# Optimization experiments

Measured on AMD Instinct MI355X. Metric: run time of the kernel, lower is better.

Reference implementation:

```python
import jax, jax.numpy as jnp
import numpy as np

B, S, D, H, HD = 2, 4096, 768, 12, 64
W = 256  # one-sided attention window (attention_window=512 // 2)
SCALE = 1.0 / np.sqrt(HD).astype(np.float32)
NEG = -1e9


def setup_inputs() -> dict:
    key = jax.random.key(0)
    ks = jax.random.split(key, 13)
    inp = {"hidden_states": jax.random.normal(ks[0], (B, S, D), dtype=jnp.float32)}
    names = ["Wq", "Wk", "Wv", "Wqg", "Wkg", "Wvg"]
    for i, n in enumerate(names):
        inp[n] = jax.random.normal(ks[1 + i], (D, D), dtype=jnp.float32) * 0.02
        inp["b" + n[1:]] = jax.random.normal(ks[7 + i], (D,), dtype=jnp.float32) * 0.02
    inp["num_global"] = 32
    return inp


def _heads(x):
    # [B,S,D] -> [B,H,S,HD]
    return x.reshape(B, S, H, HD).transpose(0, 2, 1, 3)


def longformer_attn(hidden_states, Wq, bq, Wk, bk, Wv, bv, Wqg, bqg, Wkg, bkg, Wvg, bvg, G):
    q = _heads(hidden_states @ Wq + bq) * SCALE
    k = _heads(hidden_states @ Wk + bk)
    v = _heads(hidden_states @ Wv + bv)

    nc = S // W  # number of query chunks
    # --- banded (sliding window) scores via overlapping key chunks of size 3W ---
    Qc = q.reshape(B, H, nc, W, HD)
    kpad = jnp.pad(k, ((0, 0), (0, 0), (W, W), (0, 0)))
    win_idx = jnp.arange(nc)[:, None] * W + jnp.arange(3 * W)[None, :]  # [nc, 3W]
    K3 = kpad[:, :, win_idx]  # [B,H,nc,3W,HD]
    band = jnp.einsum('bhcqd,bhckd->bhcqk', Qc, K3)  # [B,H,nc,W,3W]
    # mask: key abs position in range, and relative offset within [-W, W]
    c = jnp.arange(nc)[:, None, None]
    pq = jnp.arange(W)[None, :, None]
    e = jnp.arange(3 * W)[None, None, :]
    kabs = c * W + e - W
    valid = (kabs >= 0) & (kabs < S) & (e >= pq) & (e <= pq + 2 * W)
    band = jnp.where(valid[None, None], band, NEG).reshape(B, H, S, 3 * W)

    # --- all queries also attend to the G global keys (regular key proj) ---
    sg = jnp.einsum('bhsd,bhgd->bhsg', q, k[:, :, :G])  # [B,H,S,G]
    probs = jax.nn.softmax(jnp.concatenate([sg, band], axis=-1), axis=-1)
    pg, pb = probs[..., :G], probs[..., G:].reshape(B, H, nc, W, 3 * W)

    vpad = jnp.pad(v, ((0, 0), (0, 0), (W, W), (0, 0)))
    V3 = vpad[:, :, win_idx]  # [B,H,nc,3W,HD]
    out = jnp.einsum('bhcqk,bhckd->bhcqd', pb, V3).reshape(B, H, S, HD)
    out = out + jnp.einsum('bhsg,bhgd->bhsd', pg, v[:, :, :G])

    # --- global queries attend to ALL tokens with the *_global projections ---
    qg = _heads(hidden_states @ Wqg + bqg)[:, :, :G] * SCALE  # [B,H,G,HD]
    kgf = _heads(hidden_states @ Wkg + bkg)
    vgf = _heads(hidden_states @ Wvg + bvg)
    gp = jax.nn.softmax(jnp.einsum('bhgd,bhsd->bhgs', qg, kgf), axis=-1)
    gout = jnp.einsum('bhgs,bhsd->bhgd', gp, vgf)  # [B,H,G,HD]
    out = out.at[:, :, :G].set(gout)

    return out.transpose(0, 2, 1, 3).reshape(B, S, D)


def reference(hidden_states, Wq, bq, Wk, bk, Wv, bv, Wqg, bqg, Wkg, bkg, Wvg, bvg, num_global):
    return longformer_attn(hidden_states, Wq, bq, Wk, bk, Wv, bv, Wqg, bqg, Wkg, bkg, Wvg, bvg, int(num_global))
```

## Files before the change

### kernel.cpp

```cpp
#include <hip/hip_runtime.h>
#include <hip/hip_bf16.h>


#define DEVI __device__ __forceinline__
typedef _Float16 f16;
typedef _Float16 h4 __attribute__((ext_vector_type(4)));
typedef _Float16 f16x8 __attribute__((ext_vector_type(8)));
typedef __attribute__((ext_vector_type(4))) float float4v;

DEVI float4v mfma16(f16x8 a, f16x8 b, float4v c) {
    return __builtin_amdgcn_mfma_f32_16x16x32_f16(a, b, c, 0, 0, 0);
}

DEVI void gl_lds16(const f16* g, f16* l) {
    __builtin_amdgcn_global_load_lds(
        (const __attribute__((address_space(1))) unsigned int*)g,
        (__attribute__((address_space(3))) unsigned int*)l, 16, 0, 0);
}

__global__ __launch_bounds__(256) void prep(
    const float* __restrict__ x,
    const float* __restrict__ w0, const float* __restrict__ w1,
    const float* __restrict__ w2, const float* __restrict__ w3,
    const float* __restrict__ w4, const float* __restrict__ w5,
    f16* __restrict__ xh, f16* __restrict__ wt) {
    __shared__ float tile[64][65];
    int bid = blockIdx.x;
    if (bid < 6144) {
        int i = (bid * 256 + threadIdx.x) * 4;
        float4 v = *(const float4*)&x[i];
        h4 o = {(f16)v.x, (f16)v.y, (f16)v.z, (f16)v.w};
        *(h4*)&xh[i] = o;
    } else {
        int t = bid - 6144;
        int i = t / 144, rem = t - i * 144;
        int n0 = (rem % 12) * 64, k0 = (rem / 12) * 64;
        const float* W = (i == 0) ? w0 : (i == 1) ? w1 : (i == 2) ? w2
                       : (i == 3) ? w3 : (i == 4) ? w4 : w5;
        int tx = threadIdx.x & 63, ty = threadIdx.x >> 6;
#pragma unroll
        for (int yy = 0; yy < 64; yy += 4)
            tile[yy + ty][tx] = W[(size_t)(k0 + yy + ty) * 768 + n0 + tx];
        __syncthreads();
#pragma unroll
        for (int yy = 0; yy < 64; yy += 4)
            wt[(size_t)(i * 768 + n0 + yy + ty) * 768 + k0 + tx] = (f16)tile[tx][yy + ty];
    }
}

__global__ __launch_bounds__(256, 2) void qkv_mfma11(
    const f16* __restrict__ Xh, const f16* __restrict__ Wt,
    const float* __restrict__ b0, const float* __restrict__ b1,
    const float* __restrict__ b2, const float* __restrict__ b3,
    const float* __restrict__ b4, const float* __restrict__ b5,
    f16* __restrict__ q, f16* __restrict__ k, f16* __restrict__ vT,
    f16* __restrict__ qg, f16* __restrict__ kg, f16* __restrict__ vgT) {
    __shared__ __align__(16) char smem[73728];
    f16* As = (f16*)smem;
    f16* Bs = (f16*)(smem + 24576);
    f16* Cl = (f16*)smem;

    int tid = threadIdx.x, lane = tid & 63, wid = tid >> 6;
    int quad = lane >> 4, l15 = lane & 15;

    int L = blockIdx.x + (blockIdx.y << 6);
    int xcd = L & 7, W = L >> 3;
    int mt = xcd * 8 + (W & 7);
    int yy = W >> 3;
    int m0 = mt * 128;
    int grp = yy / 3;
    if (grp == 3 && (m0 & 4095) != 0) return;
    int nb = (yy - grp * 3) * 256;
    int wm = (wid >> 1) * 64;
    int wn = (wid & 1) * 128;
    const f16* arow0 = Xh + (size_t)m0 * 768;
    const f16* brow0 = Wt + (size_t)(grp * 768 + nb) * 768;

    float4v acc[4][8];
#pragma unroll
    for (int i = 0; i < 4; ++i)
#pragma unroll
        for (int j = 0; j < 8; ++j) acc[i][j] = (float4v){0.f, 0.f, 0.f, 0.f};

    int r0 = tid >> 2;
    int o0 = (((tid & 3) ^ ((r0 >> 1) & 3)) << 3);
    int sw8 = ((quad ^ ((l15 >> 1) & 3)) << 3);

    auto STAGE_T = [&](int kt, int buf) {
        int k0 = kt << 5;
        const f16* ag = &arow0[(size_t)r0 * 768 + k0 + o0];
        const f16* bg = &brow0[(size_t)r0 * 768 + k0 + o0];
        f16* al = As + buf * 4096 + wid * 512;
        f16* bl = Bs + buf * 8192 + wid * 512;
        gl_lds16(ag, al);
        gl_lds16(ag + (size_t)64 * 768, al + 2048);
        gl_lds16(bg, bl);
        gl_lds16(bg + (size_t)64 * 768, bl + 2048);
        gl_lds16(bg + (size_t)128 * 768, bl + 4096);
        gl_lds16(bg + (size_t)192 * 768, bl + 6144);
    };

    auto COMPUTE_T = [&](int t) {
        const f16* Ab = As + (t % 3) * 4096;
        const f16* Bb = Bs + (t % 3) * 8192;
        f16x8 af[4], bf[8];
#pragma unroll
        for (int i = 0; i < 4; ++i)
            af[i] = *(const f16x8*)&Ab[(wm + i * 16 + l15) * 32 + sw8];
#pragma unroll
        for (int j = 0; j < 8; ++j)
            bf[j] = *(const f16x8*)&Bb[(wn + j * 16 + l15) * 32 + sw8];
        __builtin_amdgcn_s_setprio(1);
#pragma unroll
        for (int i = 0; i < 4; ++i)
#pragma unroll
            for (int j = 0; j < 8; ++j)
                acc[i][j] = mfma16(af[i], bf[j], acc[i][j]);
        __builtin_amdgcn_s_setprio(0);
    };

    STAGE_T(0, 0);
    STAGE_T(1, 1);
#pragma unroll
    for (int t = 0; t < 24; ++t) {
        if (t < 23) {
            asm volatile("s_waitcnt vmcnt(6)" ::: "memory");
        } else {
            asm volatile("s_waitcnt vmcnt(0)" ::: "memory");
        }
        __builtin_amdgcn_s_barrier();
        __builtin_amdgcn_sched_barrier(0);
        if (t + 2 <= 23) STAGE_T(t + 2, (t + 2) % 3);
        COMPUTE_T(t);
    }
    __syncthreads();

    const float* Bsel = (grp == 0) ? b0 : (grp == 1) ? b1 : (grp == 2) ? b2
                      : (grp == 3) ? b3 : (grp == 4) ? b4 : b5;
    int b = m0 >> 12;
    bool tr = (grp == 2 || grp == 5);

    if (tr) {
        constexpr int CLD2 = 136;
#pragma unroll
        for (int j = 0; j < 8; ++j) {
            float bias = Bsel[nb + wn + j * 16 + l15];
#pragma unroll
            for (int i = 0; i < 4; ++i) {
                float4v a = acc[i][j];
                h4 pk = {(f16)(a[0] + bias), (f16)(a[1] + bias),
                         (f16)(a[2] + bias), (f16)(a[3] + bias)};
                *(h4*)&Cl[(wn + j * 16 + l15) * CLD2 + wm + i * 16 + quad * 4] = pk;
            }
        }
        __syncthreads();
        f16* base = (grp == 2) ? vT : vgT;
        int c = tid;
        int ncol = nb + c, h = ncol >> 6, hd = ncol & 63;
        f16* dst = &base[((size_t)((b * 12 + h) * 64 + hd)) * 4096 + (m0 & 4095)];
        const f16* src = &Cl[c * CLD2];
#pragma unroll
        for (int ii = 0; ii < 16; ++ii)
            *(f16x8*)&dst[ii * 8] = *(const f16x8*)&src[ii * 8];
    } else {
        constexpr int CLD = 264;
        float scale = (grp == 0 || grp == 3) ? 0.125f : 1.0f;
#pragma unroll
        for (int j = 0; j < 8; ++j) {
            float bias = Bsel[nb + wn + j * 16 + l15];
#pragma unroll
            for (int i = 0; i < 4; ++i) {
                float4v a = acc[i][j];
#pragma unroll
                for (int r = 0; r < 4; ++r)
                    Cl[(wm + i * 16 + quad * 4 + r) * CLD + wn + j * 16 + l15] =
                        (f16)((a[r] + bias) * scale);
            }
        }
        __syncthreads();
        int row = tid & 127, half = tid >> 7;
        int s = (m0 & 4095) + row;
        const f16* src = &Cl[row * CLD + half * 128];
        if (grp == 3) {
            if (s < 32) {
#pragma unroll
                for (int ii = 0; ii < 16; ++ii) {
                    int h = (nb >> 6) + (half << 1) + (ii >> 3), hd = (ii & 7) * 8;
                    *(f16x8*)&qg[((size_t)((b * 12 + h) * 32 + s)) * 64 + hd] =
                        *(const f16x8*)&src[ii * 8];
                }
            }
        } else {
            f16* baseb = (grp == 0) ? q : (grp == 1) ? k : kg;
#pragma unroll
            for (int ii = 0; ii < 16; ++ii) {
                int h = (nb >> 6) + (half << 1) + (ii >> 3), hd = (ii & 7) * 8;
                *(f16x8*)&baseb[((size_t)((b * 12 + h) * 4096 + s)) * 64 + hd] =
                    *(const f16x8*)&src[ii * 8];
            }
        }
    }
}

__global__ __launch_bounds__(256, 3) void band_mfma5b(
    const f16* __restrict__ q, const f16* __restrict__ k, const f16* __restrict__ vT,
    float* __restrict__ out) {
    constexpr int LDK = 72, LDV = 136, LDP = 40;
    __shared__ __align__(16) f16 Kt[128 * LDK];
    __shared__ __align__(16) f16 Vt[64 * LDV];
    __shared__ __align__(16) f16 Pt[4][32 * LDP];
    int tid = threadIdx.x, lane = tid & 63, wid = tid >> 6;
    int quad = lane >> 4, l15 = lane & 15;
    int L = blockIdx.x;
    int c = (L & 7) * 4 + ((L >> 3) & 3);
    int bh = L >> 5;
    int h = bh % 12, b = bh / 12;
    const f16* qsl = q + (size_t)(b * 12 + h) * 4096 * 64;
    const f16* ksl = k + (size_t)(b * 12 + h) * 4096 * 64;
    const f16* vsl = vT + (size_t)(b * 12 + h) * 64 * 4096;
    int q0 = c * 128;
    int pq0 = q0 + wid * 32;

    f16x8 qf[2][2];
#pragma unroll
    for (int qg = 0; qg < 2; ++qg)
#pragma unroll
        for (int ks = 0; ks < 2; ++ks)
            qf[qg][ks] = *(const f16x8*)&qsl[(size_t)(pq0 + qg * 16 + l15) * 64 +
                                             ks * 32 + quad * 8];

    float4v Ot[4][2];
#pragma unroll
    for (int dt = 0; dt < 4; ++dt)
#pragma unroll
        for (int qg = 0; qg < 2; ++qg) Ot[dt][qg] = (float4v){0.f, 0.f, 0.f, 0.f};
    float lacc[2] = {0.f, 0.f};
    f16* PW = &Pt[wid][0];

    {
#pragma unroll
        for (int jt = 0; jt < 2; ++jt) {
            f16x8 kf0 = *(const f16x8*)&ksl[(size_t)(jt * 16 + l15) * 64 + quad * 8];
            f16x8 kf1 = *(const f16x8*)&ksl[(size_t)(jt * 16 + l15) * 64 + 32 + quad * 8];
#pragma unroll
            for (int qg = 0; qg < 2; ++qg) {
                float4v sacc = (float4v){0.f, 0.f, 0.f, 0.f};
                sacc = mfma16(kf0, qf[qg][0], sacc);
                sacc = mfma16(kf1, qf[qg][1], sacc);
                float p0 = __expf(sacc[0]), p1 = __expf(sacc[1]);
                float p2 = __expf(sacc[2]), p3 = __expf(sacc[3]);
                lacc[qg] += (p0 + p1) + (p2 + p3);
                h4 pk = {(f16)p0, (f16)p1, (f16)p2, (f16)p3};
                *(h4*)&PW[(qg * 16 + l15) * LDP + jt * 16 + quad * 4] = pk;
            }
        }
        f16x8 pf0 = *(const f16x8*)&PW[l15 * LDP + quad * 8];
        f16x8 pf1 = *(const f16x8*)&PW[(16 + l15) * LDP + quad * 8];
#pragma unroll
        for (int dt = 0; dt < 4; ++dt) {
            f16x8 vf = *(const f16x8*)&vsl[(size_t)(dt * 16 + l15) * 4096 + quad * 8];
            Ot[dt][0] = mfma16(vf, pf0, Ot[dt][0]);
            Ot[dt][1] = mfma16(vf, pf1, Ot[dt][1]);
        }
    }

    for (int r = 0; r < 5; ++r) {
        int kb = q0 - 256 + r * 128;
        if (kb < 0 || kb >= 4096) continue;
        __syncthreads();
        {
            int kr = tid >> 1, ko = (tid & 1) * 32;
            const f16* ks2 = &ksl[(size_t)(kb + kr) * 64 + ko];
            f16* kd = &Kt[kr * LDK + ko];
#pragma unroll
            for (int i = 0; i < 4; ++i) *(f16x8*)&kd[i * 8] = *(const f16x8*)&ks2[i * 8];
            int vr = tid >> 2, vo = (tid & 3) * 32;
            const f16* vs2 = &vsl[(size_t)vr * 4096 + kb + vo];
            f16* vd = &Vt[vr * LDV + vo];
#pragma unroll
            for (int i = 0; i < 4; ++i) *(f16x8*)&vd[i * 8] = *(const f16x8*)&vs2[i * 8];
        }
        __syncthreads();

        if (kb + 127 < pq0 - 256 || kb > pq0 + 287) continue;

#pragma unroll
        for (int tt = 0; tt < 2; ++tt) {
            int tb = kb + tt * 64;
            if (tb + 63 < pq0 - 256 || tb > pq0 + 287) continue;
#pragma unroll
            for (int hf = 0; hf < 2; ++hf) {
#pragma unroll
                for (int jt = 0; jt < 2; ++jt) {
                    int jl = tt * 64 + hf * 32 + jt * 16;
                    f16x8 kf0 = *(const f16x8*)&Kt[(jl + l15) * LDK + quad * 8];
                    f16x8 kf1 = *(const f16x8*)&Kt[(jl + l15) * LDK + 32 + quad * 8];
                    int j0 = kb + jl;
#pragma unroll
                    for (int qg = 0; qg < 2; ++qg) {
                        int qlo = pq0 + qg * 16;
                        h4 pk = {(f16)0.f, (f16)0.f, (f16)0.f, (f16)0.f};
                        bool dead = (j0 < qlo - 271) || (j0 > qlo + 271);
                        if (!dead) {
                            float4v sacc = (float4v){0.f, 0.f, 0.f, 0.f};
                            sacc = mfma16(kf0, qf[qg][0], sacc);
                            sacc = mfma16(kf1, qf[qg][1], sacc);
                            float p[4];
                            bool full = (j0 >= qlo - 241) && (j0 <= qlo + 241);
                            if (full) {
#pragma unroll
                                for (int rr = 0; rr < 4; ++rr) p[rr] = __expf(sacc[rr]);
                            } else {
#pragma unroll
                                for (int rr = 0; rr < 4; ++rr) {
                                    int d = (j0 + quad * 4 + rr) - (qlo + l15);
                                    p[rr] = ((unsigned)(d + 256) <= 512u) ? __expf(sacc[rr]) : 0.f;
                                }
                            }
                            lacc[qg] += (p[0] + p[1]) + (p[2] + p[3]);
                            pk = (h4){(f16)p[0], (f16)p[1], (f16)p[2], (f16)p[3]};
                        }
                        *(h4*)&PW[(qg * 16 + l15) * LDP + jt * 16 + quad * 4] = pk;
                    }
                }
                f16x8 pf0 = *(const f16x8*)&PW[l15 * LDP + quad * 8];
                f16x8 pf1 = *(const f16x8*)&PW[(16 + l15) * LDP + quad * 8];
#pragma unroll
                for (int dt = 0; dt < 4; ++dt) {
                    f16x8 vf = *(const f16x8*)&Vt[(dt * 16 + l15) * LDV +
                                                  tt * 64 + hf * 32 + quad * 8];
                    Ot[dt][0] = mfma16(vf, pf0, Ot[dt][0]);
                    Ot[dt][1] = mfma16(vf, pf1, Ot[dt][1]);
                }
            }
        }
    }

#pragma unroll
    for (int qg = 0; qg < 2; ++qg) {
        float lsum = lacc[qg];
        lsum += __shfl_xor(lsum, 16);
        lsum += __shfl_xor(lsum, 32);
        float inv = 1.f / lsum;
        size_t orow = (size_t)(b * 4096 + pq0 + qg * 16 + l15) * 768 + h * 64;
#pragma unroll
        for (int dt = 0; dt < 4; ++dt) {
            float4 o4 = {Ot[dt][qg][0] * inv, Ot[dt][qg][1] * inv,
                         Ot[dt][qg][2] * inv, Ot[dt][qg][3] * inv};
            *(float4*)&out[orow + dt * 16 + quad * 4] = o4;
        }
    }
}

__global__ __launch_bounds__(256) void global_part(
    const f16* __restrict__ qg, const f16* __restrict__ kg, const f16* __restrict__ vgT,
    float* __restrict__ Opart, float* __restrict__ Lpart) {
    constexpr int LDP = 72;
    __shared__ __align__(16) f16 Pt[4][32 * LDP];
    __shared__ __align__(16) float Osh[4][64 * 32];
    __shared__ float Lsh[4][32];
    int tid = threadIdx.x, lane = tid & 63, wid = tid >> 6;
    int quad = lane >> 4, l15 = lane & 15;
    int sl = blockIdx.x & 7, bh = blockIdx.x >> 3;
    const f16* qsl = qg + (size_t)bh * 32 * 64;
    const f16* ksl = kg + (size_t)bh * 4096 * 64;
    const f16* vsl = vgT + (size_t)bh * 64 * 4096;
    int kbase = sl * 512 + wid * 128;

    f16x8 qf[2][2];
#pragma unroll
    for (int g = 0; g < 2; ++g)
#pragma unroll
        for (int ks = 0; ks < 2; ++ks)
            qf[g][ks] = *(const f16x8*)&qsl[(size_t)(g * 16 + l15) * 64 + ks * 32 + quad * 8];

    float4v Ot[4][2];
#pragma unroll
    for (int dt = 0; dt < 4; ++dt)
#pragma unroll
        for (int g = 0; g < 2; ++g) Ot[dt][g] = (float4v){0.f, 0.f, 0.f, 0.f};
    float lacc[2] = {0.f, 0.f};
    f16* PW = &Pt[wid][0];

#pragma unroll
    for (int hf = 0; hf < 2; ++hf) {
        int kh0 = kbase + hf * 64;
#pragma unroll
        for (int kt = 0; kt < 4; ++kt) {
            int jb = kh0 + kt * 16;
            f16x8 kf0 = *(const f16x8*)&ksl[(size_t)(jb + l15) * 64 + quad * 8];
            f16x8 kf1 = *(const f16x8*)&ksl[(size_t)(jb + l15) * 64 + 32 + quad * 8];
#pragma unroll
            for (int g = 0; g < 2; ++g) {
                float4v sacc = (float4v){0.f, 0.f, 0.f, 0.f};
                sacc = mfma16(kf0, qf[g][0], sacc);
                sacc = mfma16(kf1, qf[g][1], sacc);
                float p0 = __expf(sacc[0]), p1 = __expf(sacc[1]);
                float p2 = __expf(sacc[2]), p3 = __expf(sacc[3]);
                lacc[g] += (p0 + p1) + (p2 + p3);
                h4 pk = {(f16)p0, (f16)p1, (f16)p2, (f16)p3};
                *(h4*)&PW[(g * 16 + l15) * LDP + kt * 16 + quad * 4] = pk;
            }
        }
#pragma unroll
        for (int kh = 0; kh < 2; ++kh) {
            f16x8 pf0 = *(const f16x8*)&PW[l15 * LDP + kh * 32 + quad * 8];
            f16x8 pf1 = *(const f16x8*)&PW[(16 + l15) * LDP + kh * 32 + quad * 8];
#pragma unroll
            for (int dt = 0; dt < 4; ++dt) {
                f16x8 vf = *(const f16x8*)&vsl[(size_t)(dt * 16 + l15) * 4096 +
                                               kh0 + kh * 32 + quad * 8];
                Ot[dt][0] = mfma16(vf, pf0, Ot[dt][0]);
                Ot[dt][1] = mfma16(vf, pf1, Ot[dt][1]);
            }
        }
    }

#pragma unroll
    for (int g = 0; g < 2; ++g) {
        lacc[g] += __shfl_xor(lacc[g], 16);
        lacc[g] += __shfl_xor(lacc[g], 32);
    }
    if (quad == 0) { Lsh[wid][l15] = lacc[0]; Lsh[wid][16 + l15] = lacc[1]; }
#pragma unroll
    for (int dt = 0; dt < 4; ++dt)
#pragma unroll
        for (int g = 0; g < 2; ++g)
#pragma unroll
            for (int r = 0; r < 4; ++r)
                Osh[wid][(dt * 16 + quad * 4 + r) * 32 + g * 16 + l15] = Ot[dt][g][r];
    __syncthreads();
#pragma unroll
    for (int i = 0; i < 8; ++i) {
        int idx = tid + i * 256;
        int d = idx & 63, qq = idx >> 6;
        float v = Osh[0][d * 32 + qq] + Osh[1][d * 32 + qq] +
                  Osh[2][d * 32 + qq] + Osh[3][d * 32 + qq];
        Opart[(size_t)blockIdx.x * 2048 + idx] = v;
    }
    if (tid < 32)
        Lpart[blockIdx.x * 32 + tid] = Lsh[0][tid] + Lsh[1][tid] + Lsh[2][tid] + Lsh[3][tid];
}

__global__ __launch_bounds__(256) void global_reduce(
    const float* __restrict__ Opart, const float* __restrict__ Lpart,
    float* __restrict__ out) {
    __shared__ float Ls[32];
    int tid = threadIdx.x, bh = blockIdx.x;
    int b = bh / 12, h = bh % 12;
    if (tid < 32) {
        float s = 0.f;
#pragma unroll
        for (int sl = 0; sl < 8; ++sl) s += Lpart[(bh * 8 + sl) * 32 + tid];
        Ls[tid] = s;
    }
    __syncthreads();
#pragma unroll
    for (int i = 0; i < 8; ++i) {
        int idx = tid + i * 256;
        int d = idx & 63, qq = idx >> 6;
        float o = 0.f;
#pragma unroll
        for (int sl = 0; sl < 8; ++sl) o += Opart[(size_t)(bh * 8 + sl) * 2048 + idx];
        out[(size_t)(b * 4096 + qq) * 768 + h * 64 + d] = o / Ls[qq];
    }
}

extern "C" void kernel_launch(void* const* d_in, const int* in_sizes, int n_in,
                              void* d_out, int out_size, void* d_ws, size_t ws_size,
                              hipStream_t stream) {
    const float* hs = (const float*)d_in[0];
    float* outp = (float*)d_out;

    char* p = (char*)d_ws;
    const size_t SLAB = (size_t)2 * 12 * 4096 * 64 * sizeof(f16);
    f16* qb   = (f16*)(p + 0 * SLAB);
    f16* kb   = (f16*)(p + 1 * SLAB);
    f16* vtb  = (f16*)(p + 2 * SLAB);
    f16* kgb  = (f16*)(p + 3 * SLAB);
    f16* vgtb = (f16*)(p + 4 * SLAB);
    f16* qgb  = (f16*)(p + 5 * SLAB);
    char* p2  = p + 5 * SLAB + 196608;
    f16* xh   = (f16*)p2;
    f16* wt   = (f16*)(p2 + SLAB);
    char* p3  = p2 + SLAB + 7077888;
    float* Opart = (float*)p3;
    float* Lpart = (float*)(p3 + 1572864);

    prep<<<7008, 256, 0, stream>>>(
        hs,
        (const float*)d_in[1], (const float*)d_in[3], (const float*)d_in[5],
        (const float*)d_in[7], (const float*)d_in[9], (const float*)d_in[11],
        xh, wt);
    qkv_mfma11<<<dim3(64, 18), 256, 0, stream>>>(
        xh, wt,
        (const float*)d_in[2], (const float*)d_in[4], (const float*)d_in[6],
        (const float*)d_in[8], (const float*)d_in[10], (const float*)d_in[12],
        qb, kb, vtb, qgb, kgb, vgtb);
    band_mfma5b<<<768, 256, 0, stream>>>(qb, kb, vtb, outp);
    global_part<<<192, 256, 0, stream>>>(qgb, kgb, vgtb, Opart, Lpart);
    global_reduce<<<24, 256, 0, stream>>>(Opart, Lpart, outp);
}
```

Measured before the change: 227.2 us.

## Fuse band attention and global-query partial kernels into one launch

Merges the sliding-window band kernel and the global-query partial kernel into a single 960-block launch, branching on block index and sharing one LDS buffer. The aim is to save a kernel launch and let the 192 global blocks fill the tail of the band grid. The band block index mapping also changes from the interleaved chunk order to a linear one, which changes cache locality. The shared LDS allocation is sized for the larger global path (about 51 KB), which may lower band-block occupancy compared to its own smaller footprint.

```diff
diff --git a/kernel.cpp b/kernel.cpp
--- a/kernel.cpp
+++ b/kernel.cpp
@@ -202,244 +202,240 @@
     }
 }
 
-__global__ __launch_bounds__(256, 3) void band_mfma5b(
+__global__ __launch_bounds__(256, 3) void band_global(
     const f16* __restrict__ q, const f16* __restrict__ k, const f16* __restrict__ vT,
-    float* __restrict__ out) {
-    constexpr int LDK = 72, LDV = 136, LDP = 40;
-    __shared__ __align__(16) f16 Kt[128 * LDK];
-    __shared__ __align__(16) f16 Vt[64 * LDV];
-    __shared__ __align__(16) f16 Pt[4][32 * LDP];
+    const f16* __restrict__ qg, const f16* __restrict__ kg, const f16* __restrict__ vgT,
+    float* __restrict__ out, float* __restrict__ Opart, float* __restrict__ Lpart) {
+    __shared__ __align__(16) char smem[51712];
     int tid = threadIdx.x, lane = tid & 63, wid = tid >> 6;
     int quad = lane >> 4, l15 = lane & 15;
-    int L = blockIdx.x;
-    int c = (L & 7) * 4 + ((L >> 3) & 3);
-    int bh = L >> 5;
-    int h = bh % 12, b = bh / 12;
-    const f16* qsl = q + (size_t)(b * 12 + h) * 4096 * 64;
-    const f16* ksl = k + (size_t)(b * 12 + h) * 4096 * 64;
-    const f16* vsl = vT + (size_t)(b * 12 + h) * 64 * 4096;
-    int q0 = c * 128;
-    int pq0 = q0 + wid * 32;
-
-    f16x8 qf[2][2];
-#pragma unroll
-    for (int qg = 0; qg < 2; ++qg)
-#pragma unroll
-        for (int ks = 0; ks < 2; ++ks)
-            qf[qg][ks] = *(const f16x8*)&qsl[(size_t)(pq0 + qg * 16 + l15) * 64 +
-                                             ks * 32 + quad * 8];
-
-    float4v Ot[4][2];
-#pragma unroll
-    for (int dt = 0; dt < 4; ++dt)
-#pragma unroll
-        for (int qg = 0; qg < 2; ++qg) Ot[dt][qg] = (float4v){0.f, 0.f, 0.f, 0.f};
-    float lacc[2] = {0.f, 0.f};
-    f16* PW = &Pt[wid][0];
-
-    {
-#pragma unroll
-        for (int jt = 0; jt < 2; ++jt) {
-            f16x8 kf0 = *(const f16x8*)&ksl[(size_t)(jt * 16 + l15) * 64 + quad * 8];
-            f16x8 kf1 = *(const f16x8*)&ksl[(size_t)(jt * 16 + l15) * 64 + 32 + quad * 8];
-#pragma unroll
-            for (int qg = 0; qg < 2; ++qg) {
-                float4v sacc = (float4v){0.f, 0.f, 0.f, 0.f};
-                sacc = mfma16(kf0, qf[qg][0], sacc);
-                sacc = mfma16(kf1, qf[qg][1], sacc);
-                float p0 = __expf(sacc[0]), p1 = __expf(sacc[1]);
-                float p2 = __expf(sacc[2]), p3 = __expf(sacc[3]);
-                lacc[qg] += (p0 + p1) + (p2 + p3);
-                h4 pk = {(f16)p0, (f16)p1, (f16)p2, (f16)p3};
-                *(h4*)&PW[(qg * 16 + l15) * LDP + jt * 16 + quad * 4] = pk;
-            }
-        }
-        f16x8 pf0 = *(const f16x8*)&PW[l15 * LDP + quad * 8];
-        f16x8 pf1 = *(const f16x8*)&PW[(16 + l15) * LDP + quad * 8];
-#pragma unroll
-        for (int dt = 0; dt < 4; ++dt) {
-            f16x8 vf = *(const f16x8*)&vsl[(size_t)(dt * 16 + l15) * 4096 + quad * 8];
-            Ot[dt][0] = mfma16(vf, pf0, Ot[dt][0]);
-            Ot[dt][1] = mfma16(vf, pf1, Ot[dt][1]);
-        }
-    }
-
-    for (int r = 0; r < 5; ++r) {
-        int kb = q0 - 256 + r * 128;
-        if (kb < 0 || kb >= 4096) continue;
-        __syncthreads();
+
+    if (blockIdx.x < 768) {
+        constexpr int LDK = 72, LDV = 136, LDP = 40;
+        f16* Kt = (f16*)smem;
+        f16* Vt = (f16*)(smem + 18432);
+        f16* PW = (f16*)(smem + 35840) + wid * 32 * LDP;
+        int c = blockIdx.x & 31, h = (blockIdx.x >> 5) % 12, b = blockIdx.x / 384;
+        const f16* qsl = q + (size_t)(b * 12 + h) * 4096 * 64;
+        const f16* ksl = k + (size_t)(b * 12 + h) * 4096 * 64;
+        const f16* vsl = vT + (size_t)(b * 12 + h) * 64 * 4096;
+        int q0 = c * 128;
+        int pq0 = q0 + wid * 32;
+
+        f16x8 qf[2][2];
+#pragma unroll
+        for (int qg2 = 0; qg2 < 2; ++qg2)
+#pragma unroll
+            for (int ks = 0; ks < 2; ++ks)
+                qf[qg2][ks] = *(const f16x8*)&qsl[(size_t)(pq0 + qg2 * 16 + l15) * 64 +
+                                                  ks * 32 + quad * 8];
+
+        float4v Ot[4][2];
+#pragma unroll
+        for (int dt = 0; dt < 4; ++dt)
+#pragma unroll
+            for (int qg2 = 0; qg2 < 2; ++qg2) Ot[dt][qg2] = (float4v){0.f, 0.f, 0.f, 0.f};
+        float lacc[2] = {0.f, 0.f};
+
         {
-            int kr = tid >> 1, ko = (tid & 1) * 32;
-            const f16* ks2 = &ksl[(size_t)(kb + kr) * 64 + ko];
-            f16* kd = &Kt[kr * LDK + ko];
-#pragma unroll
-            for (int i = 0; i < 4; ++i) *(f16x8*)&kd[i * 8] = *(const f16x8*)&ks2[i * 8];
-            int vr = tid >> 2, vo = (tid & 3) * 32;
-            const f16* vs2 = &vsl[(size_t)vr * 4096 + kb + vo];
-            f16* vd = &Vt[vr * LDV + vo];
-#pragma unroll
-            for (int i = 0; i < 4; ++i) *(f16x8*)&vd[i * 8] = *(const f16x8*)&vs2[i * 8];
-        }
-        __syncthreads();
-
-        if (kb + 127 < pq0 - 256 || kb > pq0 + 287) continue;
-
-#pragma unroll
-        for (int tt = 0; tt < 2; ++tt) {
-            int tb = kb + tt * 64;
-            if (tb + 63 < pq0 - 256 || tb > pq0 + 287) continue;
-#pragma unroll
-            for (int hf = 0; hf < 2; ++hf) {
-#pragma unroll
-                for (int jt = 0; jt < 2; ++jt) {
-                    int jl = tt * 64 + hf * 32 + jt * 16;
-                    f16x8 kf0 = *(const f16x8*)&Kt[(jl + l15) * LDK + quad * 8];
-                    f16x8 kf1 = *(const f16x8*)&Kt[(jl + l15) * LDK + 32 + quad * 8];
-                    int j0 = kb + jl;
-#pragma unroll
-                    for (int qg = 0; qg < 2; ++qg) {
-                        int qlo = pq0 + qg * 16;
-                        h4 pk = {(f16)0.f, (f16)0.f, (f16)0.f, (f16)0.f};
-                        bool dead = (j0 < qlo - 271) || (j0 > qlo + 271);
-                        if (!dead) {
-                            float4v sacc = (float4v){0.f, 0.f, 0.f, 0.f};
-                            sacc = mfma16(kf0, qf[qg][0], sacc);
-                            sacc = mfma16(kf1, qf[qg][1], sacc);
-                            float p[4];
-                            bool full = (j0 >= qlo - 241) && (j0 <= qlo + 241);
-                            if (full) {
-#pragma unroll
-                                for (int rr = 0; rr < 4; ++rr) p[rr] = __expf(sacc[rr]);
-                            } else {
-#pragma unroll
-                                for (int rr = 0; rr < 4; ++rr) {
-                                    int d = (j0 + quad * 4 + rr) - (qlo + l15);
-                                    p[rr] = ((unsigned)(d + 256) <= 512u) ? __expf(sacc[rr]) : 0.f;
+#pragma unroll
+            for (int jt = 0; jt < 2; ++jt) {
+                f16x8 kf0 = *(const f16x8*)&ksl[(size_t)(jt * 16 + l15) * 64 + quad * 8];
+                f16x8 kf1 = *(const f16x8*)&ksl[(size_t)(jt * 16 + l15) * 64 + 32 + quad * 8];
+#pragma unroll
+                for (int qg2 = 0; qg2 < 2; ++qg2) {
+                    float4v sacc = (float4v){0.f, 0.f, 0.f, 0.f};
+                    sacc = mfma16(kf0, qf[qg2][0], sacc);
+                    sacc = mfma16(kf1, qf[qg2][1], sacc);
+                    float p0 = __expf(sacc[0]), p1 = __expf(sacc[1]);
+                    float p2 = __expf(sacc[2]), p3 = __expf(sacc[3]);
+                    lacc[qg2] += (p0 + p1) + (p2 + p3);
+                    h4 pk = {(f16)p0, (f16)p1, (f16)p2, (f16)p3};
+                    *(h4*)&PW[(qg2 * 16 + l15) * LDP + jt * 16 + quad * 4] = pk;
+                }
+            }
+            f16x8 pf0 = *(const f16x8*)&PW[l15 * LDP + quad * 8];
+            f16x8 pf1 = *(const f16x8*)&PW[(16 + l15) * LDP + quad * 8];
+#pragma unroll
+            for (int dt = 0; dt < 4; ++dt) {
+                f16x8 vf = *(const f16x8*)&vsl[(size_t)(dt * 16 + l15) * 4096 + quad * 8];
+                Ot[dt][0] = mfma16(vf, pf0, Ot[dt][0]);
+                Ot[dt][1] = mfma16(vf, pf1, Ot[dt][1]);
+            }
+        }
+
+        for (int r = 0; r < 5; ++r) {
+            int kb = q0 - 256 + r * 128;
+            if (kb < 0 || kb >= 4096) continue;
+            __syncthreads();
+            {
+                int kr = tid >> 1, ko = (tid & 1) * 32;
+                const f16* ks2 = &ksl[(size_t)(kb + kr) * 64 + ko];
+                f16* kd = &Kt[kr * LDK + ko];
+#pragma unroll
+                for (int i = 0; i < 4; ++i) *(f16x8*)&kd[i * 8] = *(const f16x8*)&ks2[i * 8];
+                int vr = tid >> 2, vo = (tid & 3) * 32;
+                const f16* vs2 = &vsl[(size_t)vr * 4096 + kb + vo];
+                f16* vd = &Vt[vr * LDV + vo];
+#pragma unroll
+                for (int i = 0; i < 4; ++i) *(f16x8*)&vd[i * 8] = *(const f16x8*)&vs2[i * 8];
+            }
+            __syncthreads();
+
+            if (kb + 127 < pq0 - 256 || kb > pq0 + 287) continue;
+
+#pragma unroll
+            for (int tt = 0; tt < 2; ++tt) {
+                int tb = kb + tt * 64;
+                if (tb + 63 < pq0 - 256 || tb > pq0 + 287) continue;
+#pragma unroll
+                for (int hf = 0; hf < 2; ++hf) {
+#pragma unroll
+                    for (int jt = 0; jt < 2; ++jt) {
+                        int jl = tt * 64 + hf * 32 + jt * 16;
+                        f16x8 kf0 = *(const f16x8*)&Kt[(jl + l15) * LDK + quad * 8];
+                        f16x8 kf1 = *(const f16x8*)&Kt[(jl + l15) * LDK + 32 + quad * 8];
+                        int j0 = kb + jl;
+#pragma unroll
+                        for (int qg2 = 0; qg2 < 2; ++qg2) {
+                            int qlo = pq0 + qg2 * 16;
+                            h4 pk = {(f16)0.f, (f16)0.f, (f16)0.f, (f16)0.f};
+                            bool dead = (j0 < qlo - 271) || (j0 > qlo + 271);
+                            if (!dead) {
+                                float4v sacc = (float4v){0.f, 0.f, 0.f, 0.f};
+                                sacc = mfma16(kf0, qf[qg2][0], sacc);
+                                sacc = mfma16(kf1, qf[qg2][1], sacc);
+                                float p[4];
+                                bool full = (j0 >= qlo - 241) && (j0 <= qlo + 241);
+                                if (full) {
+#pragma unroll
+                                    for (int rr = 0; rr < 4; ++rr) p[rr] = __expf(sacc[rr]);
+                                } else {
+#pragma unroll
+                                    for (int rr = 0; rr < 4; ++rr) {
+                                        int d = (j0 + quad * 4 + rr) - (qlo + l15);
+                                        p[rr] = ((unsigned)(d + 256) <= 512u) ? __expf(sacc[rr]) : 0.f;
+                                    }
                                 }
+                                lacc[qg2] += (p[0] + p[1]) + (p[2] + p[3]);
+                                pk = (h4){(f16)p[0], (f16)p[1], (f16)p[2], (f16)p[3]};
                             }
-                            lacc[qg] += (p[0] + p[1]) + (p[2] + p[3]);
-                            pk = (h4){(f16)p[0], (f16)p[1], (f16)p[2], (f16)p[3]};
+                            *(h4*)&PW[(qg2 * 16 + l15) * LDP + jt * 16 + quad * 4] = pk;
                         }
-                        *(h4*)&PW[(qg * 16 + l15) * LDP + jt * 16 + quad * 4] = pk;
+                    }
+                    f16x8 pf0 = *(const f16x8*)&PW[l15 * LDP + quad * 8];
+                    f16x8 pf1 = *(const f16x8*)&PW[(16 + l15) * LDP + quad * 8];
+#pragma unroll
+                    for (int dt = 0; dt < 4; ++dt) {
+                        f16x8 vf = *(const f16x8*)&Vt[(dt * 16 + l15) * LDV +
+                                                      tt * 64 + hf * 32 + quad * 8];
+                        Ot[dt][0] = mfma16(vf, pf0, Ot[dt][0]);
+                        Ot[dt][1] = mfma16(vf, pf1, Ot[dt][1]);
                     }
                 }
-                f16x8 pf0 = *(const f16x8*)&PW[l15 * LDP + quad * 8];
-                f16x8 pf1 = *(const f16x8*)&PW[(16 + l15) * LDP + quad * 8];
+            }
+        }
+
+#pragma unroll
+        for (int qg2 = 0; qg2 < 2; ++qg2) {
+            float lsum = lacc[qg2];
+            lsum += __shfl_xor(lsum, 16);
+            lsum += __shfl_xor(lsum, 32);
+            float inv = 1.f / lsum;
+            size_t orow = (size_t)(b * 4096 + pq0 + qg2 * 16 + l15) * 768 + h * 64;
+#pragma unroll
+            for (int dt = 0; dt < 4; ++dt) {
+                float4 o4 = {Ot[dt][qg2][0] * inv, Ot[dt][qg2][1] * inv,
+                             Ot[dt][qg2][2] * inv, Ot[dt][qg2][3] * inv};
+                *(float4*)&out[orow + dt * 16 + quad * 4] = o4;
+            }
+        }
+    } else {
+        constexpr int LDP = 72;
+        f16* PW = (f16*)smem + wid * 32 * LDP;
+        float* Osh = (float*)(smem + 18432);
+        float* Lsh = (float*)(smem + 18432 + 32768);
+        int bid = blockIdx.x - 768;
+        int sl = bid & 7, bh = bid >> 3;
+        const f16* qsl = qg + (size_t)bh * 32 * 64;
+        const f16* ksl = kg + (size_t)bh * 4096 * 64;
+        const f16* vsl = vgT + (size_t)bh * 64 * 4096;
+        int kbase = sl * 512 + wid * 128;
+
+        f16x8 qf[2][2];
+#pragma unroll
+        for (int g = 0; g < 2; ++g)
+#pragma unroll
+            for (int ks = 0; ks < 2; ++ks)
+                qf[g][ks] = *(const f16x8*)&qsl[(size_t)(g * 16 + l15) * 64 + ks * 32 + quad * 8];
+
+        float4v Ot[4][2];
+#pragma unroll
+        for (int dt = 0; dt < 4; ++dt)
+#pragma unroll
+            for (int g = 0; g < 2; ++g) Ot[dt][g] = (float4v){0.f, 0.f, 0.f, 0.f};
+        float lacc[2] = {0.f, 0.f};
+
+#pragma unroll
+        for (int hf = 0; hf < 2; ++hf) {
+            int kh0 = kbase + hf * 64;
+#pragma unroll
+            for (int kt = 0; kt < 4; ++kt) {
+                int jb = kh0 + kt * 16;
+                f16x8 kf0 = *(const f16x8*)&ksl[(size_t)(jb + l15) * 64 + quad * 8];
+                f16x8 kf1 = *(const f16x8*)&ksl[(size_t)(jb + l15) * 64 + 32 + quad * 8];
+#pragma unroll
+                for (int g = 0; g < 2; ++g) {
+                    float4v sacc = (float4v){0.f, 0.f, 0.f, 0.f};
+                    sacc = mfma16(kf0, qf[g][0], sacc);
+                    sacc = mfma16(kf1, qf[g][1], sacc);
+                    float p0 = __expf(sacc[0]), p1 = __expf(sacc[1]);
+                    float p2 = __expf(sacc[2]), p3 = __expf(sacc[3]);
+                    lacc[g] += (p0 + p1) + (p2 + p3);
+                    h4 pk = {(f16)p0, (f16)p1, (f16)p2, (f16)p3};
+                    *(h4*)&PW[(g * 16 + l15) * LDP + kt * 16 + quad * 4] = pk;
+                }
+            }
+#pragma unroll
+            for (int kh = 0; kh < 2; ++kh) {
+                f16x8 pf0 = *(const f16x8*)&PW[l15 * LDP + kh * 32 + quad * 8];
+                f16x8 pf1 = *(const f16x8*)&PW[(16 + l15) * LDP + kh * 32 + quad * 8];
 #pragma unroll
                 for (int dt = 0; dt < 4; ++dt) {
-                    f16x8 vf = *(const f16x8*)&Vt[(dt * 16 + l15) * LDV +
-                                                  tt * 64 + hf * 32 + quad * 8];
+                    f16x8 vf = *(const f16x8*)&vsl[(size_t)(dt * 16 + l15) * 4096 +
+                                                   kh0 + kh * 32 + quad * 8];
                     Ot[dt][0] = mfma16(vf, pf0, Ot[dt][0]);
                     Ot[dt][1] = mfma16(vf, pf1, Ot[dt][1]);
                 }
             }
         }
-    }
-
-#pragma unroll
-    for (int qg = 0; qg < 2; ++qg) {
-        float lsum = lacc[qg];
-        lsum += __shfl_xor(lsum, 16);
-        lsum += __shfl_xor(lsum, 32);
-        float inv = 1.f / lsum;
-        size_t orow = (size_t)(b * 4096 + pq0 + qg * 16 + l15) * 768 + h * 64;
-#pragma unroll
-        for (int dt = 0; dt < 4; ++dt) {
-            float4 o4 = {Ot[dt][qg][0] * inv, Ot[dt][qg][1] * inv,
-                         Ot[dt][qg][2] * inv, Ot[dt][qg][3] * inv};
-            *(float4*)&out[orow + dt * 16 + quad * 4] = o4;
-        }
-    }
-}
-
-__global__ __launch_bounds__(256) void global_part(
-    const f16* __restrict__ qg, const f16* __restrict__ kg, const f16* __restrict__ vgT,
-    float* __restrict__ Opart, float* __restrict__ Lpart) {
-    constexpr int LDP = 72;
-    __shared__ __align__(16) f16 Pt[4][32 * LDP];
-    __shared__ __align__(16) float Osh[4][64 * 32];
-    __shared__ float Lsh[4][32];
-    int tid = threadIdx.x, lane = tid & 63, wid = tid >> 6;
-    int quad = lane >> 4, l15 = lane & 15;
-    int sl = blockIdx.x & 7, bh = blockIdx.x >> 3;
-    const f16* qsl = qg + (size_t)bh * 32 * 64;
-    const f16* ksl = kg + (size_t)bh * 4096 * 64;
-    const f16* vsl = vgT + (size_t)bh * 64 * 4096;
-    int kbase = sl * 512 + wid * 128;
-
-    f16x8 qf[2][2];
-#pragma unroll
-    for (int g = 0; g < 2; ++g)
-#pragma unroll
-        for (int ks = 0; ks < 2; ++ks)
-            qf[g][ks] = *(const f16x8*)&qsl[(size_t)(g * 16 + l15) * 64 + ks * 32 + quad * 8];
-
-    float4v Ot[4][2];
-#pragma unroll
-    for (int dt = 0; dt < 4; ++dt)
-#pragma unroll
-        for (int g = 0; g < 2; ++g) Ot[dt][g] = (float4v){0.f, 0.f, 0.f, 0.f};
-    float lacc[2] = {0.f, 0.f};
-    f16* PW = &Pt[wid][0];
-
-#pragma unroll
-    for (int hf = 0; hf < 2; ++hf) {
-        int kh0 = kbase + hf * 64;
-#pragma unroll
-        for (int kt = 0; kt < 4; ++kt) {
-            int jb = kh0 + kt * 16;
-            f16x8 kf0 = *(const f16x8*)&ksl[(size_t)(jb + l15) * 64 + quad * 8];
-            f16x8 kf1 = *(const f16x8*)&ksl[(size_t)(jb + l15) * 64 + 32 + quad * 8];
-#pragma unroll
-            for (int g = 0; g < 2; ++g) {
-                float4v sacc = (float4v){0.f, 0.f, 0.f, 0.f};
-                sacc = mfma16(kf0, qf[g][0], sacc);
-                sacc = mfma16(kf1, qf[g][1], sacc);
-                float p0 = __expf(sacc[0]), p1 = __expf(sacc[1]);
-                float p2 = __expf(sacc[2]), p3 = __expf(sacc[3]);
-                lacc[g] += (p0 + p1) + (p2 + p3);
-                h4 pk = {(f16)p0, (f16)p1, (f16)p2, (f16)p3};
-                *(h4*)&PW[(g * 16 + l15) * LDP + kt * 16 + quad * 4] = pk;
-            }
-        }
-#pragma unroll
-        for (int kh = 0; kh < 2; ++kh) {
-            f16x8 pf0 = *(const f16x8*)&PW[l15 * LDP + kh * 32 + quad * 8];
-            f16x8 pf1 = *(const f16x8*)&PW[(16 + l15) * LDP + kh * 32 + quad * 8];
-#pragma unroll
-            for (int dt = 0; dt < 4; ++dt) {
-                f16x8 vf = *(const f16x8*)&vsl[(size_t)(dt * 16 + l15) * 4096 +
-                                               kh0 + kh * 32 + quad * 8];
-                Ot[dt][0] = mfma16(vf, pf0, Ot[dt][0]);
-                Ot[dt][1] = mfma16(vf, pf1, Ot[dt][1]);
-            }
-        }
-    }
-
-#pragma unroll
-    for (int g = 0; g < 2; ++g) {
-        lacc[g] += __shfl_xor(lacc[g], 16);
-        lacc[g] += __shfl_xor(lacc[g], 32);
-    }
-    if (quad == 0) { Lsh[wid][l15] = lacc[0]; Lsh[wid][16 + l15] = lacc[1]; }
-#pragma unroll
-    for (int dt = 0; dt < 4; ++dt)
-#pragma unroll
-        for (int g = 0; g < 2; ++g)
-#pragma unroll
-            for (int r = 0; r < 4; ++r)
-                Osh[wid][(dt * 16 + quad * 4 + r) * 32 + g * 16 + l15] = Ot[dt][g][r];
-    __syncthreads();
-#pragma unroll
-    for (int i = 0; i < 8; ++i) {
-        int idx = tid + i * 256;
-        int d = idx & 63, qq = idx >> 6;
-        float v = Osh[0][d * 32 + qq] + Osh[1][d * 32 + qq] +
-                  Osh[2][d * 32 + qq] + Osh[3][d * 32 + qq];
-        Opart[(size_t)blockIdx.x * 2048 + idx] = v;
-    }
-    if (tid < 32)
-        Lpart[blockIdx.x * 32 + tid] = Lsh[0][tid] + Lsh[1][tid] + Lsh[2][tid] + Lsh[3][tid];
+
+#pragma unroll
+        for (int g = 0; g < 2; ++g) {
+            lacc[g] += __shfl_xor(lacc[g], 16);
+            lacc[g] += __shfl_xor(lacc[g], 32);
+        }
+        if (quad == 0) { Lsh[wid * 32 + l15] = lacc[0]; Lsh[wid * 32 + 16 + l15] = lacc[1]; }
+#pragma unroll
+        for (int dt = 0; dt < 4; ++dt)
+#pragma unroll
+            for (int g = 0; g < 2; ++g)
+#pragma unroll
+                for (int r = 0; r < 4; ++r)
+                    Osh[wid * 2048 + (dt * 16 + quad * 4 + r) * 32 + g * 16 + l15] = Ot[dt][g][r];
+        __syncthreads();
+#pragma unroll
+        for (int i = 0; i < 8; ++i) {
+            int idx = tid + i * 256;
+            int d = idx & 63, qq = idx >> 6;
+            float v = Osh[0 * 2048 + d * 32 + qq] + Osh[1 * 2048 + d * 32 + qq] +
+                      Osh[2 * 2048 + d * 32 + qq] + Osh[3 * 2048 + d * 32 + qq];
+            Opart[(size_t)bid * 2048 + idx] = v;
+        }
+        if (tid < 32)
+            Lpart[bid * 32 + tid] = Lsh[0 * 32 + tid] + Lsh[1 * 32 + tid] +
+                                    Lsh[2 * 32 + tid] + Lsh[3 * 32 + tid];
+    }
 }
 
 __global__ __launch_bounds__(256) void global_reduce(
@@ -497,7 +493,7 @@
         (const float*)d_in[2], (const float*)d_in[4], (const float*)d_in[6],
         (const float*)d_in[8], (const float*)d_in[10], (const float*)d_in[12],
         qb, kb, vtb, qgb, kgb, vgtb);
-    band_mfma5b<<<768, 256, 0, stream>>>(qb, kb, vtb, outp);
-    global_part<<<192, 256, 0, stream>>>(qgb, kgb, vgtb, Opart, Lpart);
+    band_global<<<960, 256, 0, stream>>>(
+        qb, kb, vtb, qgb, kgb, vgtb, outp, Opart, Lpart);
     global_reduce<<<24, 256, 0, stream>>>(Opart, Lpart, outp);
 }
```

Result: faster. 220.8 us, median of 4 (-2.8%).
